# Optimization experiments

Hardware: AMD Instinct MI355X
Metric: run time of the kernel (lower is better)

Reference implementation:

```python
import jax, jax.numpy as jnp
import numpy as np

T, B, TACT, ACT, H = 512, 512, 48, 6, 200
IN2 = H + 48  # lstm2 / fc1 input size


def setup_inputs() -> dict:
    key = jax.random.key(0)
    ks = jax.random.split(key, 18)
    s = 0.05
    n = lambda k, shp: jax.random.normal(k, shp, dtype=jnp.float32) * s
    return {
        "tactiles": jax.random.normal(ks[0], (T, B, TACT), dtype=jnp.float32),
        "actions": jax.random.normal(ks[1], (T, B, ACT), dtype=jnp.float32),
        "fc0_w": n(ks[2], (48, 24)), "fc0_b": n(ks[3], (48,)),
        "l1_wih": n(ks[4], (4 * H, 48)), "l1_whh": n(ks[5], (4 * H, H)),
        "l1_bih": n(ks[6], (4 * H,)), "l1_bhh": n(ks[7], (4 * H,)),
        "l2_wih": n(ks[8], (4 * H, IN2)), "l2_whh": n(ks[9], (4 * H, H)),
        "l2_bih": n(ks[10], (4 * H,)), "l2_bhh": n(ks[11], (4 * H,)),
        "fc1_w": n(ks[12], (H, IN2)), "fc1_b": n(ks[13], (H,)),
        "fc2_w": n(ks[14], (48, H)), "fc2_b": n(ks[15], (48,)),
        "context_frames": 10,
    }


def _lstm_step(x, h, c, wih, whh, bih, bhh):
    # torch nn.LSTM gate order: i, f, g, o
    gates = x @ wih.T + h @ whh.T + bih + bhh  # [B, 4H]
    i, f, g, o = jnp.split(gates, 4, axis=-1)
    i, f, o = jax.nn.sigmoid(i), jax.nn.sigmoid(f), jax.nn.sigmoid(o)
    c_new = f * c + i * jnp.tanh(g)
    h_new = o * jnp.tanh(c_new)
    return h_new, c_new


def reference(tactiles, actions, fc0_w, fc0_b, l1_wih, l1_whh, l1_bih, l1_bhh,
              l2_wih, l2_whh, l2_bih, l2_bhh, fc1_w, fc1_b, fc2_w, fc2_b,
              context_frames):
    t_total, bsz = actions.shape[0], actions.shape[1]
    state = actions[0]  # [B, 6], fixed across steps

    def step(carry, inp):
        h1, c1, h2, c2, prev_out4 = carry
        tac, act, idx = inp
        # after context phase, feed back previous prediction
        x = jnp.where(idx >= context_frames, prev_out4, tac)  # [B, 48]
        h1, c1 = _lstm_step(x, h1, c1, l1_wih, l1_whh, l1_bih, l1_bhh)
        tiled = jnp.concatenate([state, state, act, act], axis=1)  # [B, 24]
        out0 = jax.nn.relu(tiled @ fc0_w.T + fc0_b)  # [B, 48]
        a_t = jnp.concatenate([h1, out0], axis=1)  # [B, 248]
        h2, c2 = _lstm_step(a_t, h2, c2, l2_wih, l2_whh, l2_bih, l2_bhh)
        lp = jnp.concatenate([h2, x], axis=1)  # [B, 248]
        out3 = jnp.tanh(lp @ fc1_w.T + fc1_b)  # [B, 200]
        out4 = jnp.tanh(out3 @ fc2_w.T + fc2_b)  # [B, 48]
        return (h1, c1, h2, c2, out4), out4

    z = jnp.zeros((bsz, H), tactiles.dtype)
    init = (z, z, z, z, jnp.zeros((bsz, 48), tactiles.dtype))
    xs = (tactiles[:-1], actions[1:], jnp.arange(t_total - 1))
    _, ys = jax.lax.scan(step, init, xs)  # [T-1, B, 48]
    # original returns [last_output(at idx cf-1)] + outputs(idx cf..T-2)
    return ys[context_frames - 1:]
```

## Files before the change

### kernel.cpp

```cpp
#include <hip/hip_runtime.h>

typedef __attribute__((ext_vector_type(8))) short short8;
typedef __attribute__((ext_vector_type(4))) float floatx4;

#define BB    512
#define HH    200
#define NSTEP 511
#define NG    32
#define NM    8
#define FB    25
#define GWL   116

#define OW2   0
#define OW1   (OW2 + 8*112*224)
#define OF1   (OW1 + 8*112*128)
#define OF2   (OF1 + 8*32*128)
#define OFC0  (OF2 + 48*112)
#define OB1   (OFC0 + 1152)
#define OB2   (OB1 + 896)
#define OFB1  (OB2 + 896)
#define OFLG  (OFB1 + 256)
#define OEXC  (OFLG + 768)
#define WS_TOT (OEXC + NG*3*NM*400)

__device__ __forceinline__ unsigned short f2bf(float f) {
    unsigned u = __float_as_uint(f);
    unsigned r = (u + 0x7fffu + ((u >> 16) & 1u)) >> 16;
    return (unsigned short)r;
}
__device__ __forceinline__ float sigm(float x) { return 1.0f / (1.0f + __expf(-x)); }
__device__ __forceinline__ float tanh_fast(float x) {
    float e = __expf(-2.0f * fabsf(x));
    float t = 1.0f - 2.0f * e / (1.0f + e);
    return copysignf(t, x);
}

__global__ void prep_kernel(const float* __restrict__ l1_wih, const float* __restrict__ l1_whh,
                            const float* __restrict__ l1_bih, const float* __restrict__ l1_bhh,
                            const float* __restrict__ l2_wih, const float* __restrict__ l2_whh,
                            const float* __restrict__ l2_bih, const float* __restrict__ l2_bhh,
                            const float* __restrict__ fc1_w, const float* __restrict__ fc2_w,
                            const float* __restrict__ fc0_w, unsigned* __restrict__ ws)
{
    int idx = blockIdx.x * blockDim.x + threadIdx.x;
    int stride = gridDim.x * blockDim.x;
    for (int i = idx; i < OEXC; i += stride) {
        if (i < OW1) {
            int r0 = i - OW2, m = r0 / (112*224), rem = r0 % (112*224);
            int r = rem / 224, kp = rem % 224;
            int grow = (r < 100) ? 200*(r/25) + 25*m + (r%25) : -1;
            float a = 0.f, b = 0.f;
            if (grow >= 0) {
                int k0 = 2*kp, k1 = k0 + 1;
                a = (k0 < 248) ? l2_wih[grow*248 + k0] : l2_whh[grow*HH + k0 - 248];
                b = (k1 < 248) ? l2_wih[grow*248 + k1] : l2_whh[grow*HH + k1 - 248];
            }
            ws[i] = (unsigned)f2bf(a) | ((unsigned)f2bf(b) << 16);
        } else if (i < OF1) {
            int r0 = i - OW1, m = r0 / (112*128), rem = r0 % (112*128);
            int r = rem / 128, kp = rem % 128;
            int grow = (r < 100) ? 200*(r/25) + 25*m + (r%25) : -1;
            float a = 0.f, b = 0.f;
            if (grow >= 0) {
                int k0 = 2*kp, k1 = k0 + 1;
                a = (k0 < 48) ? l1_wih[grow*48 + k0] : (k0 < 248 ? l1_whh[grow*HH + k0 - 48] : 0.f);
                b = (k1 < 48) ? l1_wih[grow*48 + k1] : (k1 < 248 ? l1_whh[grow*HH + k1 - 48] : 0.f);
            }
            ws[i] = (unsigned)f2bf(a) | ((unsigned)f2bf(b) << 16);
        } else if (i < OF2) {
            int r0 = i - OF1, m = r0 / (32*128), rem = r0 % (32*128);
            int r = rem / 128, kp = rem % 128;
            int frow = (r < 25) ? 25*m + r : -1;
            float a = 0.f, b = 0.f;
            if (frow >= 0) {
                int k0 = 2*kp, k1 = k0 + 1;
                a = (k0 < 248) ? fc1_w[frow*248 + k0] : 0.f;
                b = (k1 < 248) ? fc1_w[frow*248 + k1] : 0.f;
            }
            ws[i] = (unsigned)f2bf(a) | ((unsigned)f2bf(b) << 16);
        } else if (i < OFC0) {
            int r0 = i - OF2, n = r0 / 112, kp = r0 % 112;
            int k0 = 2*kp, k1 = k0 + 1;
            float a = (k0 < 200) ? fc2_w[n*HH + k0] : 0.f;
            float b = (k1 < 200) ? fc2_w[n*HH + k1] : 0.f;
            ws[i] = (unsigned)f2bf(a) | ((unsigned)f2bf(b) << 16);
        } else if (i < OB1) {
            int r = i - OFC0, k = r / 48, j = r % 48;
            ws[i] = __float_as_uint(fc0_w[j*24 + k]);
        } else if (i < OB2) {
            int r0 = i - OB1, m = r0 / 112, r = r0 % 112;
            int grow = (r < 100) ? 200*(r/25) + 25*m + (r%25) : -1;
            ws[i] = __float_as_uint(grow >= 0 ? l1_bih[grow] + l1_bhh[grow] : 0.f);
        } else if (i < OFB1) {
            int r0 = i - OB2, m = r0 / 112, r = r0 % 112;
            int grow = (r < 100) ? 200*(r/25) + 25*m + (r%25) : -1;
            ws[i] = __float_as_uint(grow >= 0 ? l2_bih[grow] + l2_bhh[grow] : 0.f);
        } else {
            ws[i] = 0u;
        }
    }
}

__global__ void prep_fc1b(const float* __restrict__ fc1_b, unsigned* __restrict__ ws)
{
    int i = blockIdx.x * blockDim.x + threadIdx.x;
    if (i < 256) {
        int m = i / 32, r = i % 32;
        ws[OFB1 + i] = __float_as_uint(r < 25 ? fc1_b[25*m + r] : 0.f);
    }
}

__device__ __forceinline__ void put16(short8* buf, int k, int m, unsigned short v) {
    int kt = k >> 5, kk = k & 31;
    ((unsigned short*)buf)[(((kt << 6) + m + ((kk >> 3) << 4)) << 3) + (kk & 7)] = v;
}

__global__ __launch_bounds__(1024, 4)
void lstm_sync(const float* __restrict__ tactiles, const float* __restrict__ actions,
               const float* __restrict__ fc0_b, const float* __restrict__ fc2_b,
               const int* __restrict__ ctxp, unsigned* __restrict__ wsu,
               float* __restrict__ out)
{
    const int tid  = threadIdx.x;
    const int lane = tid & 63, wave = tid >> 6;
    const int ln   = lane & 15, hi = lane >> 4;
    const int g    = blockIdx.x % NG;
    const int m    = blockIdx.x / NG;
    const int r0   = g * 16;
    const int ctx  = ctxp[0];

    const short8* ws8 = (const short8*)wsu;
    unsigned* flg = wsu + OFLG;
    float*    exc = (float*)(wsu + OEXC);

    __shared__ short8 sW1[112 * 33];
    __shared__ short8 sF1[32 * 33];
    __shared__ short8 sF2[48 * 29];
    __shared__ short8 XA1[8 * 64];
    __shared__ short8 XA2[14 * 64];
    __shared__ short8 XA3[8 * 64];
    __shared__ short8 XA4[7 * 64];
    __shared__ float gates[16 * GWL];
    __shared__ float b1s[112], b2s[112], f1bs[32], f2bs[48], f0bs[48];
    __shared__ float fc0s[24 * 48];
    __shared__ float st6[16][6], ac6[16][6];

    {
        const short8* w1b = ws8 + OW1/4 + m * 3584;
        for (int i = tid; i < 3584; i += 1024) sW1[(i >> 5) * 33 + (i & 31)] = w1b[i];
        const short8* f1b = ws8 + OF1/4 + m * 1024;
        for (int i = tid; i < 1024; i += 1024) sF1[(i >> 5) * 33 + (i & 31)] = f1b[i];
        const short8* f2b = ws8 + OF2/4;
        for (int i = tid; i < 1344; i += 1024) sF2[(i / 28) * 29 + (i % 28)] = f2b[i];
        short8 z = {0,0,0,0,0,0,0,0};
        for (int i = tid; i < 2368; i += 1024) {
            if (i < 512) XA1[i] = z;
            else if (i < 1408) XA2[i - 512] = z;
            else if (i < 1920) XA3[i - 1408] = z;
            else XA4[i - 1920] = z;
        }
    }
    short8 w2r[14];
    {
        short8 z = {0,0,0,0,0,0,0,0};
        #pragma unroll
        for (int kf = 0; kf < 14; ++kf) w2r[kf] = z;
        if (wave < 7) {
            const short8* w2b = ws8 + (size_t)m * 6272;
            const int rr = wave * 16 + ln;
            #pragma unroll
            for (int kf = 0; kf < 14; ++kf) w2r[kf] = w2b[rr * 56 + kf * 4 + hi];
        }
    }
    for (int i = tid; i < 112; i += 1024) {
        b1s[i] = __uint_as_float(wsu[OB1 + m*112 + i]);
        b2s[i] = __uint_as_float(wsu[OB2 + m*112 + i]);
    }
    if (tid < 32)  f1bs[tid] = __uint_as_float(wsu[OFB1 + m*32 + tid]);
    if (tid < 48)  { f2bs[tid] = fc2_b[tid]; f0bs[tid] = fc0_b[tid]; }
    for (int i = tid; i < 1152; i += 1024) fc0s[i] = __uint_as_float(wsu[OFC0 + i]);
    if (tid < 96) { int r = tid / 6, k = tid % 6; st6[r][k] = actions[(size_t)(r0 + r) * 6 + k]; }
    float c1r = 0.f, c2r = 0.f;
    __syncthreads();

    for (int t = 0; t < NSTEP; ++t) {
        if (t < ctx) {
            if (tid < 768) {
                int r = tid / 48, j = tid % 48;
                unsigned short xb = f2bf(tactiles[((size_t)t * BB + r0 + r) * 48 + j]);
                put16(XA1, j, r, xb);
                put16(XA3, 200 + j, r, xb);
            }
            __syncthreads();
        }

        if (wave < 7) {
            floatx4 acc = {0.f, 0.f, 0.f, 0.f};
            const int rbase = (wave * 16 + ln) * 33 + hi;
            #pragma unroll
            for (int kf = 0; kf < 8; ++kf)
                acc = __builtin_amdgcn_mfma_f32_16x16x32_bf16(XA1[(kf << 6) + lane], sW1[rbase + kf*4], acc, 0, 0, 0);
            int col = wave * 16 + ln, m0 = hi * 4;
            gates[(m0+0)*GWL + col] = acc[0];
            gates[(m0+1)*GWL + col] = acc[1];
            gates[(m0+2)*GWL + col] = acc[2];
            gates[(m0+3)*GWL + col] = acc[3];
        }
        if (tid >= 928) {
            int q = tid - 928, r = q / 6, k = q % 6;
            ac6[r][k] = actions[((size_t)(t + 1) * BB + r0 + r) * 6 + k];
        }
        __syncthreads();

        if (tid < 400) {
            int r = tid / 25, f = tid % 25;
            float gi = gates[r*GWL + f]      + b1s[f];
            float gf = gates[r*GWL + 25 + f] + b1s[25 + f];
            float gg = gates[r*GWL + 50 + f] + b1s[50 + f];
            float go = gates[r*GWL + 75 + f] + b1s[75 + f];
            float c = sigm(gf) * c1r + sigm(gi) * tanh_fast(gg);
            c1r = c;
            float h = sigm(go) * tanh_fast(c);
            unsigned short hb = f2bf(h);
            int kg = 25*m + f;
            put16(XA1, 48 + kg, r, hb);
            put16(XA2, kg, r, hb);
            __hip_atomic_store(&exc[((g*3 + 0)*NM + m)*400 + tid], h,
                               __ATOMIC_RELAXED, __HIP_MEMORY_SCOPE_AGENT);
        }
        if (tid < 768) {
            int r = tid / 48, j = tid % 48;
            float acc = f0bs[j];
            #pragma unroll
            for (int k = 0; k < 24; ++k) {
                float tv = (k < 12) ? st6[r][k % 6] : ac6[r][k % 6];
                acc += tv * fc0s[k * 48 + j];
            }
            put16(XA2, 200 + j, r, f2bf(fmaxf(acc, 0.f)));
        }
        __syncthreads();

        if (tid == 0)
            __hip_atomic_store(&flg[(g*3 + 0)*NM + m], (unsigned)(t + 1),
                               __ATOMIC_RELAXED, __HIP_MEMORY_SCOPE_AGENT);
        if (tid < 8 && tid != m) {
            while (__hip_atomic_load(&flg[(g*3 + 0)*NM + tid],
                                     __ATOMIC_RELAXED, __HIP_MEMORY_SCOPE_AGENT) != (unsigned)(t + 1))
                __builtin_amdgcn_s_sleep(1);
        }
        __syncthreads();
        for (int q = tid; q < 3200; q += 1024) {
            int mm = q / 400;
            if (mm == m) continue;
            int qq = q % 400, r = qq / 25, f = qq % 25;
            float v = __hip_atomic_load(&exc[((g*3 + 0)*NM + mm)*400 + qq],
                                        __ATOMIC_RELAXED, __HIP_MEMORY_SCOPE_AGENT);
            unsigned short hb = f2bf(v);
            int kg = 25*mm + f;
            put16(XA1, 48 + kg, r, hb);
            put16(XA2, kg, r, hb);
        }
        __syncthreads();

        if (wave < 7) {
            floatx4 acc = {0.f, 0.f, 0.f, 0.f};
            #pragma unroll
            for (int kf = 0; kf < 14; ++kf)
                acc = __builtin_amdgcn_mfma_f32_16x16x32_bf16(XA2[(kf << 6) + lane], w2r[kf], acc, 0, 0, 0);
            int col = wave * 16 + ln, m0 = hi * 4;
            gates[(m0+0)*GWL + col] = acc[0];
            gates[(m0+1)*GWL + col] = acc[1];
            gates[(m0+2)*GWL + col] = acc[2];
            gates[(m0+3)*GWL + col] = acc[3];
        }
        __syncthreads();

        if (tid < 400) {
            int r = tid / 25, f = tid % 25;
            float gi = gates[r*GWL + f]      + b2s[f];
            float gf = gates[r*GWL + 25 + f] + b2s[25 + f];
            float gg = gates[r*GWL + 50 + f] + b2s[50 + f];
            float go = gates[r*GWL + 75 + f] + b2s[75 + f];
            float c = sigm(gf) * c2r + sigm(gi) * tanh_fast(gg);
            c2r = c;
            float h = sigm(go) * tanh_fast(c);
            unsigned short hb = f2bf(h);
            int kg = 25*m + f;
            put16(XA2, 248 + kg, r, hb);
            put16(XA3, kg, r, hb);
            __hip_atomic_store(&exc[((g*3 + 1)*NM + m)*400 + tid], h,
                               __ATOMIC_RELAXED, __HIP_MEMORY_SCOPE_AGENT);
        }
        __syncthreads();

        if (tid == 0)
            __hip_atomic_store(&flg[(g*3 + 1)*NM + m], (unsigned)(t + 1),
                               __ATOMIC_RELAXED, __HIP_MEMORY_SCOPE_AGENT);
        if (tid < 8 && tid != m) {
            while (__hip_atomic_load(&flg[(g*3 + 1)*NM + tid],
                                     __ATOMIC_RELAXED, __HIP_MEMORY_SCOPE_AGENT) != (unsigned)(t + 1))
                __builtin_amdgcn_s_sleep(1);
        }
        __syncthreads();
        for (int q = tid; q < 3200; q += 1024) {
            int mm = q / 400;
            if (mm == m) continue;
            int qq = q % 400, r = qq / 25, f = qq % 25;
            float v = __hip_atomic_load(&exc[((g*3 + 1)*NM + mm)*400 + qq],
                                        __ATOMIC_RELAXED, __HIP_MEMORY_SCOPE_AGENT);
            unsigned short hb = f2bf(v);
            int kg = 25*mm + f;
            put16(XA2, 248 + kg, r, hb);
            put16(XA3, kg, r, hb);
        }
        __syncthreads();

        if (wave < 2) {
            floatx4 acc = {0.f, 0.f, 0.f, 0.f};
            const int rbase = (wave * 16 + ln) * 33 + hi;
            #pragma unroll
            for (int kf = 0; kf < 8; ++kf)
                acc = __builtin_amdgcn_mfma_f32_16x16x32_bf16(XA3[(kf << 6) + lane], sF1[rbase + kf*4], acc, 0, 0, 0);
            int col = wave * 16 + ln, m0 = hi * 4;
            gates[(m0+0)*GWL + col] = acc[0];
            gates[(m0+1)*GWL + col] = acc[1];
            gates[(m0+2)*GWL + col] = acc[2];
            gates[(m0+3)*GWL + col] = acc[3];
        }
        __syncthreads();

        if (tid < 400) {
            int r = tid / 25, f = tid % 25;
            float v = tanh_fast(gates[r*GWL + f] + f1bs[f]);
            put16(XA4, 25*m + f, r, f2bf(v));
            __hip_atomic_store(&exc[((g*3 + 2)*NM + m)*400 + tid], v,
                               __ATOMIC_RELAXED, __HIP_MEMORY_SCOPE_AGENT);
        }
        __syncthreads();

        if (tid == 0)
            __hip_atomic_store(&flg[(g*3 + 2)*NM + m], (unsigned)(t + 1),
                               __ATOMIC_RELAXED, __HIP_MEMORY_SCOPE_AGENT);
        if (tid < 8 && tid != m) {
            while (__hip_atomic_load(&flg[(g*3 + 2)*NM + tid],
                                     __ATOMIC_RELAXED, __HIP_MEMORY_SCOPE_AGENT) != (unsigned)(t + 1))
                __builtin_amdgcn_s_sleep(1);
        }
        __syncthreads();
        for (int q = tid; q < 3200; q += 1024) {
            int mm = q / 400;
            if (mm == m) continue;
            int qq = q % 400, r = qq / 25, f = qq % 25;
            float v = __hip_atomic_load(&exc[((g*3 + 2)*NM + mm)*400 + qq],
                                        __ATOMIC_RELAXED, __HIP_MEMORY_SCOPE_AGENT);
            put16(XA4, 25*mm + f, r, f2bf(v));
        }
        __syncthreads();

        if (wave < 3) {
            floatx4 acc = {0.f, 0.f, 0.f, 0.f};
            const int rbase = (wave * 16 + ln) * 29 + hi;
            #pragma unroll
            for (int kf = 0; kf < 7; ++kf)
                acc = __builtin_amdgcn_mfma_f32_16x16x32_bf16(XA4[(kf << 6) + lane], sF2[rbase + kf*4], acc, 0, 0, 0);
            int col = wave * 16 + ln, m0 = hi * 4;
            gates[(m0+0)*GWL + col] = acc[0];
            gates[(m0+1)*GWL + col] = acc[1];
            gates[(m0+2)*GWL + col] = acc[2];
            gates[(m0+3)*GWL + col] = acc[3];
        }
        __syncthreads();

        if (tid < 768) {
            int r = tid / 48, j = tid % 48;
            float v = tanh_fast(gates[r*GWL + j] + f2bs[j]);
            unsigned short xb = f2bf(v);
            put16(XA1, j, r, xb);
            put16(XA3, 200 + j, r, xb);
            if (m == 0 && t >= ctx - 1)
                out[((size_t)(t - (ctx - 1)) * BB + r0 + r) * 48 + j] = v;
        }
        __syncthreads();
    }
}

extern "C" void kernel_launch(void* const* d_in, const int* in_sizes, int n_in,
                              void* d_out, int out_size, void* d_ws, size_t ws_size,
                              hipStream_t stream)
{
    const float* tactiles = (const float*)d_in[0];
    const float* actions  = (const float*)d_in[1];
    const float* fc0_w    = (const float*)d_in[2];
    const float* fc0_b    = (const float*)d_in[3];
    const float* l1_wih   = (const float*)d_in[4];
    const float* l1_whh   = (const float*)d_in[5];
    const float* l1_bih   = (const float*)d_in[6];
    const float* l1_bhh   = (const float*)d_in[7];
    const float* l2_wih   = (const float*)d_in[8];
    const float* l2_whh   = (const float*)d_in[9];
    const float* l2_bih   = (const float*)d_in[10];
    const float* l2_bhh   = (const float*)d_in[11];
    const float* fc1_w    = (const float*)d_in[12];
    const float* fc1_b    = (const float*)d_in[13];
    const float* fc2_w    = (const float*)d_in[14];
    const float* fc2_b    = (const float*)d_in[15];
    const int*   ctxp     = (const int*)d_in[16];
    unsigned* ws = (unsigned*)d_ws;
    float* out = (float*)d_out;

    hipLaunchKernelGGL(prep_kernel, dim3(512), dim3(256), 0, stream,
                       l1_wih, l1_whh, l1_bih, l1_bhh,
                       l2_wih, l2_whh, l2_bih, l2_bhh,
                       fc1_w, fc2_w, fc0_w, ws);
    hipLaunchKernelGGL(prep_fc1b, dim3(1), dim3(256), 0, stream, fc1_b, ws);
    hipLaunchKernelGGL(lstm_sync, dim3(256), dim3(1024), 0, stream,
                       tactiles, actions, fc0_b, fc2_b, ctxp, ws, out);
}
```

Before: 3.984 ms.

## Split fc1 along K across blocks and merge partial sums to drop a grid barrier

fc1 is no longer split by output rows, which needed a third cross-block flag exchange per timestep. Each block now computes partial fc1 sums over its own 25 h2 columns, with block 0 also covering the x columns. The partials go to global memory with the same exchange as h2, and every block reduces all 8 partials to form the full fc1 output locally before fc2. This removes one inter-block synchronisation per step, at the cost of more global traffic and redundant reduction and fc2 work in every block. The fc2 weights move from LDS into registers.

```diff
diff --git a/kernel.cpp b/kernel.cpp
--- a/kernel.cpp
+++ b/kernel.cpp
@@ -8,20 +8,23 @@
 #define NSTEP 511
 #define NG    32
 #define NM    8
-#define FB    25
 #define GWL   116
+#define EX2S  3840
 
 #define OW2   0
 #define OW1   (OW2 + 8*112*224)
-#define OF1   (OW1 + 8*112*128)
-#define OF2   (OF1 + 8*32*128)
+#define OF1P  (OW1 + 8*112*128)
+#define OF2   (OF1P + 8*208*52)
 #define OFC0  (OF2 + 48*112)
 #define OB1   (OFC0 + 1152)
 #define OB2   (OB1 + 896)
-#define OFB1  (OB2 + 896)
-#define OFLG  (OFB1 + 256)
-#define OEXC  (OFLG + 768)
-#define WS_TOT (OEXC + NG*3*NM*400)
+#define OFLG  (OB2 + 896)
+#define OEX1  (OFLG + 512)
+#define OEX2  (OEX1 + NG*NM*400)
+#define WS_TOT (OEX2 + NG*NM*EX2S)
+
+#define AST(p, v) __hip_atomic_store((p), (v), __ATOMIC_RELAXED, __HIP_MEMORY_SCOPE_AGENT)
+#define ALD(p)    __hip_atomic_load((p), __ATOMIC_RELAXED, __HIP_MEMORY_SCOPE_AGENT)
 
 __device__ __forceinline__ unsigned short f2bf(float f) {
     unsigned u = __float_as_uint(f);
@@ -44,7 +47,7 @@
 {
     int idx = blockIdx.x * blockDim.x + threadIdx.x;
     int stride = gridDim.x * blockDim.x;
-    for (int i = idx; i < OEXC; i += stride) {
+    for (int i = idx; i < OEX1; i += stride) {
         if (i < OW1) {
             int r0 = i - OW2, m = r0 / (112*224), rem = r0 % (112*224);
             int r = rem / 224, kp = rem % 224;
@@ -56,7 +59,7 @@
                 b = (k1 < 248) ? l2_wih[grow*248 + k1] : l2_whh[grow*HH + k1 - 248];
             }
             ws[i] = (unsigned)f2bf(a) | ((unsigned)f2bf(b) << 16);
-        } else if (i < OF1) {
+        } else if (i < OF1P) {
             int r0 = i - OW1, m = r0 / (112*128), rem = r0 % (112*128);
             int r = rem / 128, kp = rem % 128;
             int grow = (r < 100) ? 200*(r/25) + 25*m + (r%25) : -1;
@@ -68,14 +71,15 @@
             }
             ws[i] = (unsigned)f2bf(a) | ((unsigned)f2bf(b) << 16);
         } else if (i < OF2) {
-            int r0 = i - OF1, m = r0 / (32*128), rem = r0 % (32*128);
-            int r = rem / 128, kp = rem % 128;
-            int frow = (r < 25) ? 25*m + r : -1;
+            int r0 = i - OF1P, m = r0 / (208*52), rem = r0 % (208*52);
+            int row = rem / 52, w = rem % 52;
             float a = 0.f, b = 0.f;
-            if (frow >= 0) {
-                int k0 = 2*kp, k1 = k0 + 1;
-                a = (k0 < 248) ? fc1_w[frow*248 + k0] : 0.f;
-                b = (k1 < 248) ? fc1_w[frow*248 + k1] : 0.f;
+            if (row < 200) {
+                int k0 = 2*w, k1 = k0 + 1;
+                if (k0 < 25) a = fc1_w[row*248 + 25*m + k0];
+                else if (k0 >= 32 && k0 < 80 && m == 0) a = fc1_w[row*248 + 200 + (k0-32)];
+                if (k1 < 25) b = fc1_w[row*248 + 25*m + k1];
+                else if (k1 >= 32 && k1 < 80 && m == 0) b = fc1_w[row*248 + 200 + (k1-32)];
             }
             ws[i] = (unsigned)f2bf(a) | ((unsigned)f2bf(b) << 16);
         } else if (i < OFC0) {
@@ -91,7 +95,7 @@
             int r0 = i - OB1, m = r0 / 112, r = r0 % 112;
             int grow = (r < 100) ? 200*(r/25) + 25*m + (r%25) : -1;
             ws[i] = __float_as_uint(grow >= 0 ? l1_bih[grow] + l1_bhh[grow] : 0.f);
-        } else if (i < OFB1) {
+        } else if (i < OFLG) {
             int r0 = i - OB2, m = r0 / 112, r = r0 % 112;
             int grow = (r < 100) ? 200*(r/25) + 25*m + (r%25) : -1;
             ws[i] = __float_as_uint(grow >= 0 ? l2_bih[grow] + l2_bhh[grow] : 0.f);
@@ -101,15 +105,6 @@
     }
 }
 
-__global__ void prep_fc1b(const float* __restrict__ fc1_b, unsigned* __restrict__ ws)
-{
-    int i = blockIdx.x * blockDim.x + threadIdx.x;
-    if (i < 256) {
-        int m = i / 32, r = i % 32;
-        ws[OFB1 + i] = __float_as_uint(r < 25 ? fc1_b[25*m + r] : 0.f);
-    }
-}
-
 __device__ __forceinline__ void put16(short8* buf, int k, int m, unsigned short v) {
     int kt = k >> 5, kk = k & 31;
     ((unsigned short*)buf)[(((kt << 6) + m + ((kk >> 3) << 4)) << 3) + (kk & 7)] = v;
@@ -117,9 +112,9 @@
 
 __global__ __launch_bounds__(1024, 4)
 void lstm_sync(const float* __restrict__ tactiles, const float* __restrict__ actions,
-               const float* __restrict__ fc0_b, const float* __restrict__ fc2_b,
-               const int* __restrict__ ctxp, unsigned* __restrict__ wsu,
-               float* __restrict__ out)
+               const float* __restrict__ fc0_b, const float* __restrict__ fc1_b,
+               const float* __restrict__ fc2_b, const int* __restrict__ ctxp,
+               unsigned* __restrict__ wsu, float* __restrict__ out)
 {
     const int tid  = threadIdx.x;
     const int lane = tid & 63, wave = tid >> 6;
@@ -131,52 +126,58 @@
 
     const short8* ws8 = (const short8*)wsu;
     unsigned* flg = wsu + OFLG;
-    float*    exc = (float*)(wsu + OEXC);
+    float*    ex1 = (float*)(wsu + OEX1);
+    float*    ex2 = (float*)(wsu + OEX2);
 
     __shared__ short8 sW1[112 * 33];
-    __shared__ short8 sF1[32 * 33];
-    __shared__ short8 sF2[48 * 29];
+    __shared__ short8 sF1p[208 * 13];
     __shared__ short8 XA1[8 * 64];
     __shared__ short8 XA2[14 * 64];
-    __shared__ short8 XA3[8 * 64];
+    __shared__ short8 XA3p[3 * 64];
     __shared__ short8 XA4[7 * 64];
     __shared__ float gates[16 * GWL];
-    __shared__ float b1s[112], b2s[112], f1bs[32], f2bs[48], f0bs[48];
+    __shared__ float b1s[112], b2s[112], f1bs[200], f2bs[48], f0bs[48];
     __shared__ float fc0s[24 * 48];
     __shared__ float st6[16][6], ac6[16][6];
 
     {
         const short8* w1b = ws8 + OW1/4 + m * 3584;
         for (int i = tid; i < 3584; i += 1024) sW1[(i >> 5) * 33 + (i & 31)] = w1b[i];
-        const short8* f1b = ws8 + OF1/4 + m * 1024;
-        for (int i = tid; i < 1024; i += 1024) sF1[(i >> 5) * 33 + (i & 31)] = f1b[i];
-        const short8* f2b = ws8 + OF2/4;
-        for (int i = tid; i < 1344; i += 1024) sF2[(i / 28) * 29 + (i % 28)] = f2b[i];
+        const short8* f1b = ws8 + OF1P/4 + m * 2704;
+        for (int i = tid; i < 2704; i += 1024) sF1p[i] = f1b[i];
         short8 z = {0,0,0,0,0,0,0,0};
-        for (int i = tid; i < 2368; i += 1024) {
+        for (int i = tid; i < 2048; i += 1024) {
             if (i < 512) XA1[i] = z;
             else if (i < 1408) XA2[i - 512] = z;
-            else if (i < 1920) XA3[i - 1408] = z;
-            else XA4[i - 1920] = z;
-        }
-    }
-    short8 w2r[14];
+            else if (i < 1600) XA3p[i - 1408] = z;
+            else XA4[i - 1600] = z;
+        }
+    }
+    short8 w2r[14], f2r[7];
     {
         short8 z = {0,0,0,0,0,0,0,0};
         #pragma unroll
         for (int kf = 0; kf < 14; ++kf) w2r[kf] = z;
+        #pragma unroll
+        for (int kf = 0; kf < 7; ++kf) f2r[kf] = z;
         if (wave < 7) {
             const short8* w2b = ws8 + (size_t)m * 6272;
             const int rr = wave * 16 + ln;
             #pragma unroll
             for (int kf = 0; kf < 14; ++kf) w2r[kf] = w2b[rr * 56 + kf * 4 + hi];
         }
+        if (wave < 3) {
+            const short8* f2b = ws8 + OF2/4;
+            const int rr = wave * 16 + ln;
+            #pragma unroll
+            for (int kf = 0; kf < 7; ++kf) f2r[kf] = f2b[rr * 28 + kf * 4 + hi];
+        }
     }
     for (int i = tid; i < 112; i += 1024) {
         b1s[i] = __uint_as_float(wsu[OB1 + m*112 + i]);
         b2s[i] = __uint_as_float(wsu[OB2 + m*112 + i]);
     }
-    if (tid < 32)  f1bs[tid] = __uint_as_float(wsu[OFB1 + m*32 + tid]);
+    if (tid < 200) f1bs[tid] = fc1_b[tid];
     if (tid < 48)  { f2bs[tid] = fc2_b[tid]; f0bs[tid] = fc0_b[tid]; }
     for (int i = tid; i < 1152; i += 1024) fc0s[i] = __uint_as_float(wsu[OFC0 + i]);
     if (tid < 96) { int r = tid / 6, k = tid % 6; st6[r][k] = actions[(size_t)(r0 + r) * 6 + k]; }
@@ -189,7 +190,7 @@
                 int r = tid / 48, j = tid % 48;
                 unsigned short xb = f2bf(tactiles[((size_t)t * BB + r0 + r) * 48 + j]);
                 put16(XA1, j, r, xb);
-                put16(XA3, 200 + j, r, xb);
+                put16(XA3p, 32 + j, r, xb);
             }
             __syncthreads();
         }
@@ -225,8 +226,7 @@
             int kg = 25*m + f;
             put16(XA1, 48 + kg, r, hb);
             put16(XA2, kg, r, hb);
-            __hip_atomic_store(&exc[((g*3 + 0)*NM + m)*400 + tid], h,
-                               __ATOMIC_RELAXED, __HIP_MEMORY_SCOPE_AGENT);
+            AST(&ex1[(g*NM + m)*400 + tid], h);
         }
         if (tid < 768) {
             int r = tid / 48, j = tid % 48;
@@ -240,12 +240,9 @@
         }
         __syncthreads();
 
-        if (tid == 0)
-            __hip_atomic_store(&flg[(g*3 + 0)*NM + m], (unsigned)(t + 1),
-                               __ATOMIC_RELAXED, __HIP_MEMORY_SCOPE_AGENT);
+        if (tid == 0) AST(&flg[(g*2 + 0)*NM + m], (unsigned)(t + 1));
         if (tid < 8 && tid != m) {
-            while (__hip_atomic_load(&flg[(g*3 + 0)*NM + tid],
-                                     __ATOMIC_RELAXED, __HIP_MEMORY_SCOPE_AGENT) != (unsigned)(t + 1))
+            while (ALD(&flg[(g*2 + 0)*NM + tid]) != (unsigned)(t + 1))
                 __builtin_amdgcn_s_sleep(1);
         }
         __syncthreads();
@@ -253,8 +250,7 @@
             int mm = q / 400;
             if (mm == m) continue;
             int qq = q % 400, r = qq / 25, f = qq % 25;
-            float v = __hip_atomic_load(&exc[((g*3 + 0)*NM + mm)*400 + qq],
-                                        __ATOMIC_RELAXED, __HIP_MEMORY_SCOPE_AGENT);
+            float v = ALD(&ex1[(g*NM + mm)*400 + qq]);
             unsigned short hb = f2bf(v);
             int kg = 25*mm + f;
             put16(XA1, 48 + kg, r, hb);
@@ -285,20 +281,30 @@
             c2r = c;
             float h = sigm(go) * tanh_fast(c);
             unsigned short hb = f2bf(h);
-            int kg = 25*m + f;
-            put16(XA2, 248 + kg, r, hb);
-            put16(XA3, kg, r, hb);
-            __hip_atomic_store(&exc[((g*3 + 1)*NM + m)*400 + tid], h,
-                               __ATOMIC_RELAXED, __HIP_MEMORY_SCOPE_AGENT);
-        }
-        __syncthreads();
-
-        if (tid == 0)
-            __hip_atomic_store(&flg[(g*3 + 1)*NM + m], (unsigned)(t + 1),
-                               __ATOMIC_RELAXED, __HIP_MEMORY_SCOPE_AGENT);
+            put16(XA2, 248 + 25*m + f, r, hb);
+            put16(XA3p, f, r, hb);
+            AST(&ex2[(g*NM + m)*EX2S + tid], h);
+        }
+        __syncthreads();
+
+        if (wave < 13) {
+            floatx4 acc = {0.f, 0.f, 0.f, 0.f};
+            const int rbase = (wave * 16 + ln) * 13 + hi;
+            #pragma unroll
+            for (int kf = 0; kf < 3; ++kf)
+                acc = __builtin_amdgcn_mfma_f32_16x16x32_bf16(XA3p[(kf << 6) + lane], sF1p[rbase + kf*4], acc, 0, 0, 0);
+            int n = wave * 16 + ln, m0 = hi * 4;
+            float* dst = ex2 + (g*NM + m)*EX2S + 400 + n*16 + m0;
+            AST(&dst[0], acc[0]);
+            AST(&dst[1], acc[1]);
+            AST(&dst[2], acc[2]);
+            AST(&dst[3], acc[3]);
+        }
+        __syncthreads();
+
+        if (tid == 0) AST(&flg[(g*2 + 1)*NM + m], (unsigned)(t + 1));
         if (tid < 8 && tid != m) {
-            while (__hip_atomic_load(&flg[(g*3 + 1)*NM + tid],
-                                     __ATOMIC_RELAXED, __HIP_MEMORY_SCOPE_AGENT) != (unsigned)(t + 1))
+            while (ALD(&flg[(g*2 + 1)*NM + tid]) != (unsigned)(t + 1))
                 __builtin_amdgcn_s_sleep(1);
         }
         __syncthreads();
@@ -306,21 +312,24 @@
             int mm = q / 400;
             if (mm == m) continue;
             int qq = q % 400, r = qq / 25, f = qq % 25;
-            float v = __hip_atomic_load(&exc[((g*3 + 1)*NM + mm)*400 + qq],
-                                        __ATOMIC_RELAXED, __HIP_MEMORY_SCOPE_AGENT);
-            unsigned short hb = f2bf(v);
-            int kg = 25*mm + f;
-            put16(XA2, 248 + kg, r, hb);
-            put16(XA3, kg, r, hb);
-        }
-        __syncthreads();
-
-        if (wave < 2) {
+            float v = ALD(&ex2[(g*NM + mm)*EX2S + qq]);
+            put16(XA2, 248 + 25*mm + f, r, f2bf(v));
+        }
+        for (int q = tid; q < 3200; q += 1024) {
+            int r = q & 15, n = q >> 4;
+            float s = f1bs[n];
+            #pragma unroll
+            for (int mm = 0; mm < 8; ++mm)
+                s += ALD(&ex2[(g*NM + mm)*EX2S + 400 + q]);
+            put16(XA4, n, r, f2bf(tanh_fast(s)));
+        }
+        __syncthreads();
+
+        if (wave < 3) {
             floatx4 acc = {0.f, 0.f, 0.f, 0.f};
-            const int rbase = (wave * 16 + ln) * 33 + hi;
-            #pragma unroll
-            for (int kf = 0; kf < 8; ++kf)
-                acc = __builtin_amdgcn_mfma_f32_16x16x32_bf16(XA3[(kf << 6) + lane], sF1[rbase + kf*4], acc, 0, 0, 0);
+            #pragma unroll
+            for (int kf = 0; kf < 7; ++kf)
+                acc = __builtin_amdgcn_mfma_f32_16x16x32_bf16(XA4[(kf << 6) + lane], f2r[kf], acc, 0, 0, 0);
             int col = wave * 16 + ln, m0 = hi * 4;
             gates[(m0+0)*GWL + col] = acc[0];
             gates[(m0+1)*GWL + col] = acc[1];
@@ -329,54 +338,12 @@
         }
         __syncthreads();
 
-        if (tid < 400) {
-            int r = tid / 25, f = tid % 25;
-            float v = tanh_fast(gates[r*GWL + f] + f1bs[f]);
-            put16(XA4, 25*m + f, r, f2bf(v));
-            __hip_atomic_store(&exc[((g*3 + 2)*NM + m)*400 + tid], v,
-                               __ATOMIC_RELAXED, __HIP_MEMORY_SCOPE_AGENT);
-        }
-        __syncthreads();
-
-        if (tid == 0)
-            __hip_atomic_store(&flg[(g*3 + 2)*NM + m], (unsigned)(t + 1),
-                               __ATOMIC_RELAXED, __HIP_MEMORY_SCOPE_AGENT);
-        if (tid < 8 && tid != m) {
-            while (__hip_atomic_load(&flg[(g*3 + 2)*NM + tid],
-                                     __ATOMIC_RELAXED, __HIP_MEMORY_SCOPE_AGENT) != (unsigned)(t + 1))
-                __builtin_amdgcn_s_sleep(1);
-        }
-        __syncthreads();
-        for (int q = tid; q < 3200; q += 1024) {
-            int mm = q / 400;
-            if (mm == m) continue;
-            int qq = q % 400, r = qq / 25, f = qq % 25;
-            float v = __hip_atomic_load(&exc[((g*3 + 2)*NM + mm)*400 + qq],
-                                        __ATOMIC_RELAXED, __HIP_MEMORY_SCOPE_AGENT);
-            put16(XA4, 25*mm + f, r, f2bf(v));
-        }
-        __syncthreads();
-
-        if (wave < 3) {
-            floatx4 acc = {0.f, 0.f, 0.f, 0.f};
-            const int rbase = (wave * 16 + ln) * 29 + hi;
-            #pragma unroll
-            for (int kf = 0; kf < 7; ++kf)
-                acc = __builtin_amdgcn_mfma_f32_16x16x32_bf16(XA4[(kf << 6) + lane], sF2[rbase + kf*4], acc, 0, 0, 0);
-            int col = wave * 16 + ln, m0 = hi * 4;
-            gates[(m0+0)*GWL + col] = acc[0];
-            gates[(m0+1)*GWL + col] = acc[1];
-            gates[(m0+2)*GWL + col] = acc[2];
-            gates[(m0+3)*GWL + col] = acc[3];
-        }
-        __syncthreads();
-
         if (tid < 768) {
             int r = tid / 48, j = tid % 48;
             float v = tanh_fast(gates[r*GWL + j] + f2bs[j]);
             unsigned short xb = f2bf(v);
             put16(XA1, j, r, xb);
-            put16(XA3, 200 + j, r, xb);
+            put16(XA3p, 32 + j, r, xb);
             if (m == 0 && t >= ctx - 1)
                 out[((size_t)(t - (ctx - 1)) * BB + r0 + r) * 48 + j] = v;
         }
@@ -412,7 +379,6 @@
                        l1_wih, l1_whh, l1_bih, l1_bhh,
                        l2_wih, l2_whh, l2_bih, l2_bhh,
                        fc1_w, fc2_w, fc0_w, ws);
-    hipLaunchKernelGGL(prep_fc1b, dim3(1), dim3(256), 0, stream, fc1_b, ws);
     hipLaunchKernelGGL(lstm_sync, dim3(256), dim3(1024), 0, stream,
-                       tactiles, actions, fc0_b, fc2_b, ctxp, ws, out);
-}
+                       tactiles, actions, fc0_b, fc1_b, fc2_b, ctxp, ws, out);
+}
```

After: 9.028 ms. 2.27x slower.
